# Kernel optimization log

Measured on AMD Instinct MI355X. Metric: run time of the kernel, lower is better.

## Reference

```python
import jax, jax.numpy as jnp
import numpy as np

LN_EPS = 1e-5
ATTN_THRESH = 0.0005


def _layernorm(x, g, b):
    mu = jnp.mean(x, axis=-1, keepdims=True)
    var = jnp.mean((x - mu) ** 2, axis=-1, keepdims=True)
    return (x - mu) / jnp.sqrt(var + LN_EPS) * g + b


def setup_inputs() -> dict:
    key = jax.random.key(0)
    ks = jax.random.split(key, 10)
    B, P, X, C = 4, 1024, 8192, 1024
    return {
        "feat": jax.random.normal(ks[0], (B, P, C), dtype=jnp.float32),
        "mem_k": jax.random.normal(ks[1], (B, X, C), dtype=jnp.float32),
        "mem_v": jax.random.normal(ks[2], (B, X, C), dtype=jnp.float32),
        "mem_c": jax.random.uniform(ks[3], (B, X, 1), dtype=jnp.float32),
        "mem_attn": jnp.zeros((B, X, 1), dtype=jnp.float32),
        "g_q": jax.random.uniform(ks[4], (C,), dtype=jnp.float32, minval=0.5, maxval=1.5),
        "b_q": jax.random.normal(ks[5], (C,), dtype=jnp.float32) * 0.02,
        "g_k": jax.random.uniform(ks[6], (C,), dtype=jnp.float32, minval=0.5, maxval=1.5),
        "b_k": jax.random.normal(ks[7], (C,), dtype=jnp.float32) * 0.02,
        "g_v": jax.random.uniform(ks[8], (C,), dtype=jnp.float32, minval=0.5, maxval=1.5),
        "b_v": jax.random.normal(ks[9], (C,), dtype=jnp.float32) * 0.02,
    }


def reference(feat, mem_k, mem_v, mem_c, mem_attn, g_q, b_q, g_k, b_k, g_v, b_v):
    # SpatialMemory.memory_read with res=True
    C = feat.shape[-1]
    q = _layernorm(feat, g_q, b_q)                      # [B,P,C]
    k = _layernorm(mem_k, g_k, b_k)                     # [B,X,C]
    affinity = jnp.einsum('bpc,bxc->bpx', q, k)
    affinity = affinity / jnp.sqrt(jnp.asarray(C, jnp.float32))
    # confidence scaling: mem_c viewed as [B,1,X]
    affinity = affinity * jnp.swapaxes(mem_c, 1, 2)
    attn = jax.nn.softmax(affinity, axis=-1)            # [B,P,X]
    # threshold sparsify + renormalize
    attn = jnp.where(attn < ATTN_THRESH, jnp.zeros((), attn.dtype), attn)
    attn = attn / jnp.sum(attn, axis=-1, keepdims=True)
    v = _layernorm(mem_v, g_v, b_v)                     # [B,X,C]
    out = jnp.einsum('bpx,bxc->bpc', attn, v) + feat    # residual
    return out
```

## Files before the change

kernel.cpp:

```cpp
#include <hip/hip_runtime.h>

typedef __attribute__((ext_vector_type(8))) _Float16 half8;
typedef __attribute__((ext_vector_type(4))) _Float16 half4v;
typedef __attribute__((ext_vector_type(4))) float f32x4;

__device__ __forceinline__ void gll16(const void* g, void* l) {
  __builtin_amdgcn_global_load_lds(
      (const __attribute__((address_space(1))) unsigned int*)g,
      (__attribute__((address_space(3))) unsigned int*)l, 16, 0, 0);
}

__device__ __forceinline__ float h2f(unsigned short hb) {
  _Float16 h;
  __builtin_memcpy(&h, &hb, 2);
  return (float)h;
}

__global__ __launch_bounds__(256) void ln_cast_f16(
    const float* __restrict__ x, const float* __restrict__ g,
    const float* __restrict__ b, _Float16* __restrict__ y) {
  const int C = 1024;
  size_t row = blockIdx.x;
  int t = threadIdx.x;
  const float4* xr = (const float4*)(x + row * C);
  float4 v = xr[t];
  float s = v.x + v.y + v.z + v.w;
  float s2 = v.x * v.x + v.y * v.y + v.z * v.z + v.w * v.w;
#pragma unroll
  for (int off = 1; off < 64; off <<= 1) {
    s += __shfl_xor(s, off, 64);
    s2 += __shfl_xor(s2, off, 64);
  }
  __shared__ float ps[4], ps2[4];
  int wave = t >> 6, lane = t & 63;
  if (lane == 0) { ps[wave] = s; ps2[wave] = s2; }
  __syncthreads();
  s = ps[0] + ps[1] + ps[2] + ps[3];
  s2 = ps2[0] + ps2[1] + ps2[2] + ps2[3];
  float mu = s * (1.0f / C);
  float var = s2 * (1.0f / C) - mu * mu;
  float rstd = rsqrtf(var + 1e-5f);
  float4 gv = ((const float4*)g)[t];
  float4 bv = ((const float4*)b)[t];
  half4v o;
  o.x = (_Float16)((v.x - mu) * rstd * gv.x + bv.x);
  o.y = (_Float16)((v.y - mu) * rstd * gv.y + bv.y);
  o.z = (_Float16)((v.z - mu) * rstd * gv.z + bv.z);
  o.w = (_Float16)((v.w - mu) * rstd * gv.w + bv.w);
  ((half4v*)(y + row * C))[t] = o;
}

__global__ __launch_bounds__(512) void gemm_qk_f16(
    const _Float16* __restrict__ A,
    const _Float16* __restrict__ Bm,
    _Float16* __restrict__ Sm,
    const float* __restrict__ conf)
{
  const int M = 1024, N = 8192, K = 1024;
  int bz = blockIdx.z;
  const _Float16* Ab = A + (size_t)bz * M * K;
  const _Float16* Bb = Bm + (size_t)bz * N * K;
  _Float16* Sb = Sm + (size_t)bz * M * N;

  __shared__ _Float16 lA[256 * 32];
  __shared__ _Float16 lB[128 * 32];

  int tid = threadIdx.x;
  int wave = tid >> 6, lane = tid & 63;
  int wm = wave >> 1, wn = wave & 1;
  int m0 = blockIdx.y * 256, n0 = blockIdx.x * 128;

  f32x4 acc[4][4];
  f32x4 zero = {0.f, 0.f, 0.f, 0.f};
#pragma unroll
  for (int i = 0; i < 4; ++i)
#pragma unroll
    for (int j = 0; j < 4; ++j) acc[i][j] = zero;

  int rA0 = tid & 255, kgA0 = tid >> 8;
  int rA1 = rA0, kgA1 = kgA0 + 2;
  int rB = tid & 127, kgB = tid >> 7;
  const _Float16* gA0 = Ab + (size_t)(m0 + rA0) * K + kgA0 * 8;
  const _Float16* gA1 = Ab + (size_t)(m0 + rA1) * K + kgA1 * 8;
  const _Float16* gB0 = Bb + (size_t)(n0 + rB) * K + kgB * 8;
  _Float16* dA0 = &lA[kgA0 * 2048 + rA0 * 8];
  _Float16* dA1 = &lA[kgA1 * 2048 + rA1 * 8];
  _Float16* dB0 = &lB[kgB * 1024 + rB * 8];

  int kg = lane >> 4, lr = lane & 15;

  for (int k0 = 0; k0 < K; k0 += 32) {
    __syncthreads();
    gll16(gA0 + k0, dA0);
    gll16(gA1 + k0, dA1);
    gll16(gB0 + k0, dB0);
    __syncthreads();
    half8 af[4], bfr[4];
#pragma unroll
    for (int t = 0; t < 4; ++t) {
      int m = wm * 64 + t * 16 + lr;
      af[t] = *(const half8*)&lA[kg * 2048 + m * 8];
      int n = wn * 64 + t * 16 + lr;
      bfr[t] = *(const half8*)&lB[kg * 1024 + n * 8];
    }
#pragma unroll
    for (int t = 0; t < 4; ++t)
#pragma unroll
      for (int u = 0; u < 4; ++u)
        acc[t][u] = __builtin_amdgcn_mfma_f32_16x16x32_f16(af[t], bfr[u], acc[t][u], 0, 0, 0);
  }

  int cq = lane >> 4, cn = lane & 15;
  const float* cb = conf + (size_t)bz * N;
#pragma unroll
  for (int u = 0; u < 4; ++u) {
    int gn = n0 + wn * 64 + u * 16 + cn;
    float cs = 0.03125f * cb[gn];
#pragma unroll
    for (int t = 0; t < 4; ++t) {
      int gm = m0 + wm * 64 + t * 16 + cq * 4;
#pragma unroll
      for (int r = 0; r < 4; ++r)
        Sb[(size_t)(gm + r) * N + gn] = (_Float16)(acc[t][u][r] * cs);
    }
  }
}

__global__ __launch_bounds__(256) void softmax_compact(
    const _Float16* __restrict__ S, unsigned* __restrict__ entries,
    int* __restrict__ counts) {
  const int X = 8192;
  size_t row = blockIdx.x;
  const half8* sr = (const half8*)(S + row * X);
  int t = threadIdx.x;
  int wave = t >> 6, lane = t & 63;
  __shared__ float sh[4];
  __shared__ int scnt;

  float v[32];
#pragma unroll
  for (int j = 0; j < 4; ++j) {
    half8 h = sr[t + j * 256];
#pragma unroll
    for (int c = 0; c < 8; ++c) v[j * 8 + c] = (float)h[c];
  }

  float m = -1e30f;
#pragma unroll
  for (int i = 0; i < 32; ++i) m = fmaxf(m, v[i]);
#pragma unroll
  for (int off = 1; off < 64; off <<= 1) m = fmaxf(m, __shfl_xor(m, off, 64));
  if (lane == 0) sh[wave] = m;
  __syncthreads();
  m = fmaxf(fmaxf(sh[0], sh[1]), fmaxf(sh[2], sh[3]));
  __syncthreads();

  float l = 0.f;
#pragma unroll
  for (int i = 0; i < 32; ++i) {
    v[i] = __expf(v[i] - m);
    l += v[i];
  }
#pragma unroll
  for (int off = 1; off < 64; off <<= 1) l += __shfl_xor(l, off, 64);
  if (lane == 0) sh[wave] = l;
  __syncthreads();
  l = sh[0] + sh[1] + sh[2] + sh[3];
  __syncthreads();

  float thr = 0.0005f * l;
  float ks = 0.f;
#pragma unroll
  for (int i = 0; i < 32; ++i) {
    v[i] = (v[i] >= thr) ? v[i] : 0.f;
    ks += v[i];
  }
#pragma unroll
  for (int off = 1; off < 64; off <<= 1) ks += __shfl_xor(ks, off, 64);
  if (lane == 0) sh[wave] = ks;
  __syncthreads();
  if (t == 0) scnt = 0;
  __syncthreads();
  ks = sh[0] + sh[1] + sh[2] + sh[3];

  float inv = 1.0f / ks;
  unsigned* er = entries + row * 2048;
#pragma unroll
  for (int j = 0; j < 4; ++j) {
#pragma unroll
    for (int c = 0; c < 8; ++c) {
      float val = v[j * 8 + c];
      if (val > 0.f) {
        int pos = atomicAdd(&scnt, 1);
        _Float16 h = (_Float16)(val * inv);
        unsigned short hb;
        __builtin_memcpy(&hb, &h, 2);
        er[pos] = ((unsigned)((t + j * 256) * 8 + c) << 16) | hb;
      }
    }
  }
  __syncthreads();
  if (t == 0) counts[row] = scnt;
}

__global__ __launch_bounds__(512) void gather_pv(
    const unsigned* __restrict__ entries, const int* __restrict__ counts,
    const _Float16* __restrict__ v16, const float* __restrict__ feat,
    float* __restrict__ out) {
  const int X = 8192, C = 1024;
  int row = blockIdx.x;
  int b = row >> 10;
  int t = threadIdx.x;
  int s = t >> 7;
  int c = (t & 127) * 8;

  __shared__ unsigned se[2048];
  __shared__ float red[4][1024];

  int cnt = counts[row];
  const unsigned* er = entries + (size_t)row * 2048;
  for (int i = t; i < cnt; i += 512) se[i] = er[i];
  __syncthreads();

  const _Float16* vb = v16 + (size_t)b * X * C;
  float a0 = 0, a1 = 0, a2 = 0, a3 = 0, a4 = 0, a5 = 0, a6 = 0, a7 = 0;
#pragma unroll 4
  for (int j = s; j < cnt; j += 4) {
    unsigned e = se[j];
    int x = e >> 16;
    float w = h2f((unsigned short)(e & 0xffff));
    half8 vv = *(const half8*)(vb + (size_t)x * C + c);
    a0 += w * (float)vv[0]; a1 += w * (float)vv[1];
    a2 += w * (float)vv[2]; a3 += w * (float)vv[3];
    a4 += w * (float)vv[4]; a5 += w * (float)vv[5];
    a6 += w * (float)vv[6]; a7 += w * (float)vv[7];
  }
  float* rp = &red[s][c];
  rp[0] = a0; rp[1] = a1; rp[2] = a2; rp[3] = a3;
  rp[4] = a4; rp[5] = a5; rp[6] = a6; rp[7] = a7;
  __syncthreads();

  int p = t * 2;
  float2 f = *(const float2*)(feat + (size_t)row * C + p);
  float2 o;
  o.x = red[0][p] + red[1][p] + red[2][p] + red[3][p] + f.x;
  o.y = red[0][p + 1] + red[1][p + 1] + red[2][p + 1] + red[3][p + 1] + f.y;
  *(float2*)(out + (size_t)row * C + p) = o;
}

extern "C" void kernel_launch(void* const* d_in, const int* in_sizes, int n_in,
                              void* d_out, int out_size, void* d_ws, size_t ws_size,
                              hipStream_t stream) {
  const int B = 4, P = 1024, X = 8192, C = 1024;
  const float* feat  = (const float*)d_in[0];
  const float* mem_k = (const float*)d_in[1];
  const float* mem_v = (const float*)d_in[2];
  const float* mem_c = (const float*)d_in[3];
  const float* g_q = (const float*)d_in[5];
  const float* b_q = (const float*)d_in[6];
  const float* g_k = (const float*)d_in[7];
  const float* b_k = (const float*)d_in[8];
  const float* g_v = (const float*)d_in[9];
  const float* b_v = (const float*)d_in[10];

  char* ws = (char*)d_ws;
  const size_t MB = 1024 * 1024;
  _Float16* q16 = (_Float16*)(ws + 0);
  _Float16* k16 = (_Float16*)(ws + 8 * MB);
  _Float16* v16 = (_Float16*)(ws + 72 * MB);
  _Float16* S   = (_Float16*)(ws + 136 * MB);
  unsigned* entries = (unsigned*)(ws + 200 * MB);
  int*      counts  = (int*)(ws + 232 * MB);

  ln_cast_f16<<<B * P, 256, 0, stream>>>(feat, g_q, b_q, q16);
  ln_cast_f16<<<B * X, 256, 0, stream>>>(mem_k, g_k, b_k, k16);
  ln_cast_f16<<<B * X, 256, 0, stream>>>(mem_v, g_v, b_v, v16);
  gemm_qk_f16<<<dim3(X / 128, P / 256, B), 512, 0, stream>>>(q16, k16, S, mem_c);
  softmax_compact<<<B * P, 256, 0, stream>>>(S, entries, counts);
  gather_pv<<<B * P, 512, 0, stream>>>(entries, counts, v16, feat, (float*)d_out);
}
```

Baseline: 538.3 us.

## Quantize V to int8 per row and triple-buffer the QK GEMM

V is now layer-normalized and quantized to int8 with a per-row scale, and the sparse gather reads int8 rows with 8 waves per block instead of fp16 rows. This halves the V memory traffic in both the cast and the gather. The QK GEMM moves to 128x128 tiles with 256 threads and a three-stage global-to-LDS pipeline using explicit waitcnt and barriers, replacing the double-sync single-buffer loop. Int8 V adds quantization error to the output.

```diff
diff --git a/kernel.cpp b/kernel.cpp
--- a/kernel.cpp
+++ b/kernel.cpp
@@ -50,25 +50,72 @@
   ((half4v*)(y + row * C))[t] = o;
 }
 
-__global__ __launch_bounds__(512) void gemm_qk_f16(
+__global__ __launch_bounds__(256) void ln_cast_i8(
+    const float* __restrict__ x, const float* __restrict__ g,
+    const float* __restrict__ b, char* __restrict__ y,
+    float* __restrict__ yscale) {
+  const int C = 1024;
+  size_t row = blockIdx.x;
+  int t = threadIdx.x;
+  const float4* xr = (const float4*)(x + row * C);
+  float4 v = xr[t];
+  float s = v.x + v.y + v.z + v.w;
+  float s2 = v.x * v.x + v.y * v.y + v.z * v.z + v.w * v.w;
+#pragma unroll
+  for (int off = 1; off < 64; off <<= 1) {
+    s += __shfl_xor(s, off, 64);
+    s2 += __shfl_xor(s2, off, 64);
+  }
+  __shared__ float ps[4], ps2[4], pm[4];
+  int wave = t >> 6, lane = t & 63;
+  if (lane == 0) { ps[wave] = s; ps2[wave] = s2; }
+  __syncthreads();
+  s = ps[0] + ps[1] + ps[2] + ps[3];
+  s2 = ps2[0] + ps2[1] + ps2[2] + ps2[3];
+  float mu = s * (1.0f / C);
+  float var = s2 * (1.0f / C) - mu * mu;
+  float rstd = rsqrtf(var + 1e-5f);
+  float4 gv = ((const float4*)g)[t];
+  float4 bv = ((const float4*)b)[t];
+  float o0 = (v.x - mu) * rstd * gv.x + bv.x;
+  float o1 = (v.y - mu) * rstd * gv.y + bv.y;
+  float o2 = (v.z - mu) * rstd * gv.z + bv.z;
+  float o3 = (v.w - mu) * rstd * gv.w + bv.w;
+  float mx = fmaxf(fmaxf(fabsf(o0), fabsf(o1)), fmaxf(fabsf(o2), fabsf(o3)));
+#pragma unroll
+  for (int off = 1; off < 64; off <<= 1) mx = fmaxf(mx, __shfl_xor(mx, off, 64));
+  if (lane == 0) pm[wave] = mx;
+  __syncthreads();
+  mx = fmaxf(fmaxf(pm[0], pm[1]), fmaxf(pm[2], pm[3]));
+  mx = fmaxf(mx, 1e-20f);
+  float inv = 127.0f / mx;
+  int q0 = (int)rintf(o0 * inv), q1 = (int)rintf(o1 * inv);
+  int q2 = (int)rintf(o2 * inv), q3 = (int)rintf(o3 * inv);
+  unsigned pk = ((unsigned)(q0 & 0xff)) | ((unsigned)(q1 & 0xff) << 8) |
+                ((unsigned)(q2 & 0xff) << 16) | ((unsigned)(q3 & 0xff) << 24);
+  ((unsigned*)(y + row * C))[t] = pk;
+  if (t == 0) yscale[row] = mx * (1.0f / 127.0f);
+}
+
+__global__ __launch_bounds__(256) void gemm_qk_pipe(
     const _Float16* __restrict__ A,
     const _Float16* __restrict__ Bm,
     _Float16* __restrict__ Sm,
     const float* __restrict__ conf)
 {
-  const int M = 1024, N = 8192, K = 1024;
+  const int N = 8192, K = 1024, NSTG = 32;
   int bz = blockIdx.z;
-  const _Float16* Ab = A + (size_t)bz * M * K;
-  const _Float16* Bb = Bm + (size_t)bz * N * K;
-  _Float16* Sb = Sm + (size_t)bz * M * N;
-
-  __shared__ _Float16 lA[256 * 32];
-  __shared__ _Float16 lB[128 * 32];
+  const _Float16* Ab = A + (size_t)bz * 1024 * K;
+  const _Float16* Bb = Bm + (size_t)bz * (size_t)N * K;
+  _Float16* Sb = Sm + (size_t)bz * 1024 * N;
+
+  __shared__ _Float16 lA[3 * 4096];
+  __shared__ _Float16 lB[3 * 4096];
 
   int tid = threadIdx.x;
   int wave = tid >> 6, lane = tid & 63;
   int wm = wave >> 1, wn = wave & 1;
-  int m0 = blockIdx.y * 256, n0 = blockIdx.x * 128;
+  int m0 = blockIdx.y * 128, n0 = blockIdx.x * 128;
 
   f32x4 acc[4][4];
   f32x4 zero = {0.f, 0.f, 0.f, 0.f};
@@ -77,37 +124,52 @@
 #pragma unroll
     for (int j = 0; j < 4; ++j) acc[i][j] = zero;
 
-  int rA0 = tid & 255, kgA0 = tid >> 8;
-  int rA1 = rA0, kgA1 = kgA0 + 2;
-  int rB = tid & 127, kgB = tid >> 7;
-  const _Float16* gA0 = Ab + (size_t)(m0 + rA0) * K + kgA0 * 8;
-  const _Float16* gA1 = Ab + (size_t)(m0 + rA1) * K + kgA1 * 8;
-  const _Float16* gB0 = Bb + (size_t)(n0 + rB) * K + kgB * 8;
-  _Float16* dA0 = &lA[kgA0 * 2048 + rA0 * 8];
-  _Float16* dA1 = &lA[kgA1 * 2048 + rA1 * 8];
-  _Float16* dB0 = &lB[kgB * 1024 + rB * 8];
+  int rS = tid & 127, kg0 = tid >> 7, kg1 = kg0 + 2;
+  const _Float16* gA0 = Ab + (size_t)(m0 + rS) * K + kg0 * 8;
+  const _Float16* gA1 = Ab + (size_t)(m0 + rS) * K + kg1 * 8;
+  const _Float16* gB0 = Bb + (size_t)(n0 + rS) * K + kg0 * 8;
+  const _Float16* gB1 = Bb + (size_t)(n0 + rS) * K + kg1 * 8;
+  int d0 = kg0 * 1024 + rS * 8;
+  int d1 = kg1 * 1024 + rS * 8;
+
+  gll16(gA0, &lA[d0]); gll16(gA1, &lA[d1]);
+  gll16(gB0, &lB[d0]); gll16(gB1, &lB[d1]);
+  gll16(gA0 + 32, &lA[4096 + d0]); gll16(gA1 + 32, &lA[4096 + d1]);
+  gll16(gB0 + 32, &lB[4096 + d0]); gll16(gB1 + 32, &lB[4096 + d1]);
 
   int kg = lane >> 4, lr = lane & 15;
-
-  for (int k0 = 0; k0 < K; k0 += 32) {
-    __syncthreads();
-    gll16(gA0 + k0, dA0);
-    gll16(gA1 + k0, dA1);
-    gll16(gB0 + k0, dB0);
-    __syncthreads();
+  int bfc = 0;
+  int bfi = 2;
+
+  for (int k = 0; k < NSTG; ++k) {
+    if (k <= NSTG - 3)
+      __builtin_amdgcn_s_waitcnt(0xF74);
+    else
+      __builtin_amdgcn_s_waitcnt(0xF70);
+    __builtin_amdgcn_s_barrier();
+    __builtin_amdgcn_sched_barrier(0);
+    if (k <= NSTG - 3) {
+      int kk = (k + 2) * 32;
+      int bo = bfi * 4096;
+      gll16(gA0 + kk, &lA[bo + d0]); gll16(gA1 + kk, &lA[bo + d1]);
+      gll16(gB0 + kk, &lB[bo + d0]); gll16(gB1 + kk, &lB[bo + d1]);
+    }
+    const _Float16* la = &lA[bfc * 4096];
+    const _Float16* lb = &lB[bfc * 4096];
     half8 af[4], bfr[4];
 #pragma unroll
     for (int t = 0; t < 4; ++t) {
-      int m = wm * 64 + t * 16 + lr;
-      af[t] = *(const half8*)&lA[kg * 2048 + m * 8];
-      int n = wn * 64 + t * 16 + lr;
-      bfr[t] = *(const half8*)&lB[kg * 1024 + n * 8];
+      af[t] = *(const half8*)&la[kg * 1024 + (wm * 64 + t * 16 + lr) * 8];
+      bfr[t] = *(const half8*)&lb[kg * 1024 + (wn * 64 + t * 16 + lr) * 8];
     }
 #pragma unroll
     for (int t = 0; t < 4; ++t)
 #pragma unroll
       for (int u = 0; u < 4; ++u)
         acc[t][u] = __builtin_amdgcn_mfma_f32_16x16x32_f16(af[t], bfr[u], acc[t][u], 0, 0, 0);
+    __builtin_amdgcn_sched_barrier(0);
+    bfc = (bfc == 2) ? 0 : bfc + 1;
+    bfi = (bfi == 2) ? 0 : bfi + 1;
   }
 
   int cq = lane >> 4, cn = lane & 15;
@@ -203,48 +265,64 @@
   if (t == 0) counts[row] = scnt;
 }
 
-__global__ __launch_bounds__(512) void gather_pv(
+__device__ __forceinline__ void acc4(float* a, unsigned w, float wt) {
+  a[0] += wt * (float)(signed char)(w & 0xff);
+  a[1] += wt * (float)(signed char)((w >> 8) & 0xff);
+  a[2] += wt * (float)(signed char)((w >> 16) & 0xff);
+  a[3] += wt * (float)(signed char)(w >> 24);
+}
+
+__global__ __launch_bounds__(512) void gather_pv_i8(
     const unsigned* __restrict__ entries, const int* __restrict__ counts,
-    const _Float16* __restrict__ v16, const float* __restrict__ feat,
-    float* __restrict__ out) {
+    const char* __restrict__ v8, const float* __restrict__ vscale,
+    const float* __restrict__ feat, float* __restrict__ out) {
   const int X = 8192, C = 1024;
   int row = blockIdx.x;
   int b = row >> 10;
   int t = threadIdx.x;
-  int s = t >> 7;
-  int c = (t & 127) * 8;
+  int s = t >> 6;
+  int lane = t & 63;
+  int c = lane * 16;
 
   __shared__ unsigned se[2048];
-  __shared__ float red[4][1024];
+  __shared__ float red[8][1028];
 
   int cnt = counts[row];
   const unsigned* er = entries + (size_t)row * 2048;
   for (int i = t; i < cnt; i += 512) se[i] = er[i];
   __syncthreads();
 
-  const _Float16* vb = v16 + (size_t)b * X * C;
-  float a0 = 0, a1 = 0, a2 = 0, a3 = 0, a4 = 0, a5 = 0, a6 = 0, a7 = 0;
-#pragma unroll 4
-  for (int j = s; j < cnt; j += 4) {
+  const char* vb = v8 + (size_t)b * X * C;
+  const float* sb = vscale + (size_t)b * X;
+  float a[16];
+#pragma unroll
+  for (int i = 0; i < 16; ++i) a[i] = 0.f;
+
+#pragma unroll 2
+  for (int j = s; j < cnt; j += 8) {
     unsigned e = se[j];
     int x = e >> 16;
-    float w = h2f((unsigned short)(e & 0xffff));
-    half8 vv = *(const half8*)(vb + (size_t)x * C + c);
-    a0 += w * (float)vv[0]; a1 += w * (float)vv[1];
-    a2 += w * (float)vv[2]; a3 += w * (float)vv[3];
-    a4 += w * (float)vv[4]; a5 += w * (float)vv[5];
-    a6 += w * (float)vv[6]; a7 += w * (float)vv[7];
+    float w = h2f((unsigned short)(e & 0xffff)) * sb[x];
+    uint4 pv = *(const uint4*)(vb + (size_t)x * C + c);
+    acc4(a + 0, pv.x, w);
+    acc4(a + 4, pv.y, w);
+    acc4(a + 8, pv.z, w);
+    acc4(a + 12, pv.w, w);
   }
   float* rp = &red[s][c];
-  rp[0] = a0; rp[1] = a1; rp[2] = a2; rp[3] = a3;
-  rp[4] = a4; rp[5] = a5; rp[6] = a6; rp[7] = a7;
+#pragma unroll
+  for (int i = 0; i < 16; ++i) rp[i] = a[i];
   __syncthreads();
 
   int p = t * 2;
   float2 f = *(const float2*)(feat + (size_t)row * C + p);
-  float2 o;
-  o.x = red[0][p] + red[1][p] + red[2][p] + red[3][p] + f.x;
-  o.y = red[0][p + 1] + red[1][p + 1] + red[2][p + 1] + red[3][p + 1] + f.y;
+  float o0 = f.x, o1 = f.y;
+#pragma unroll
+  for (int ss = 0; ss < 8; ++ss) {
+    o0 += red[ss][p];
+    o1 += red[ss][p + 1];
+  }
+  float2 o = {o0, o1};
   *(float2*)(out + (size_t)row * C + p) = o;
 }
 
@@ -267,15 +345,17 @@
   const size_t MB = 1024 * 1024;
   _Float16* q16 = (_Float16*)(ws + 0);
   _Float16* k16 = (_Float16*)(ws + 8 * MB);
-  _Float16* v16 = (_Float16*)(ws + 72 * MB);
-  _Float16* S   = (_Float16*)(ws + 136 * MB);
-  unsigned* entries = (unsigned*)(ws + 200 * MB);
-  int*      counts  = (int*)(ws + 232 * MB);
+  _Float16* S   = (_Float16*)(ws + 72 * MB);
+  char*     v8  = (char*)(ws + 136 * MB);
+  float* vscale = (float*)(ws + 168 * MB);
+  unsigned* entries = (unsigned*)(ws + 169 * MB);
+  int*      counts  = (int*)(ws + 201 * MB);
 
   ln_cast_f16<<<B * P, 256, 0, stream>>>(feat, g_q, b_q, q16);
   ln_cast_f16<<<B * X, 256, 0, stream>>>(mem_k, g_k, b_k, k16);
-  ln_cast_f16<<<B * X, 256, 0, stream>>>(mem_v, g_v, b_v, v16);
-  gemm_qk_f16<<<dim3(X / 128, P / 256, B), 512, 0, stream>>>(q16, k16, S, mem_c);
+  ln_cast_i8<<<B * X, 256, 0, stream>>>(mem_v, g_v, b_v, v8, vscale);
+  gemm_qk_pipe<<<dim3(X / 128, P / 128, B), 256, 0, stream>>>(q16, k16, S, mem_c);
   softmax_compact<<<B * P, 256, 0, stream>>>(S, entries, counts);
-  gather_pv<<<B * P, 512, 0, stream>>>(entries, counts, v16, feat, (float*)d_out);
-}
+  gather_pv_i8<<<B * P, 512, 0, stream>>>(entries, counts, v8, vscale, feat,
+                                          (float*)d_out);
+}
```

Measured after the change: 529.6 us. About the same (-1.6%).
